# Performance work log

Hardware: AMD Instinct MI355X
Metric: run time of the kernel (lower is better)

Reference implementation:

```python
import jax, jax.numpy as jnp
import numpy as np

B, S, D, U, A = 8, 2048, 1024, 1024, 4  # batch, seq, input_dim, units, n_activations


def setup_inputs() -> dict:
    key = jax.random.key(0)
    ks = jax.random.split(key, 6)
    scale_w = (6.0 / (D + U)) ** 0.5  # glorot_uniform
    scale_wf = (6.0 / (U + A)) ** 0.5
    scale_wa = (6.0 / (D + A)) ** 0.5
    return {
        "x": jax.random.normal(ks[0], (B, S, D), dtype=jnp.float32),
        "w": jax.random.uniform(ks[1], (D, U), jnp.float32, -scale_w, scale_w),
        "b": jnp.zeros((U,), jnp.float32),
        "wf": jax.random.uniform(ks[2], (U, A), jnp.float32, -scale_wf, scale_wf),
        "bf": jnp.zeros((U, A), jnp.float32),
        "w_att": jax.random.uniform(ks[3], (D, A), jnp.float32, -scale_wa, scale_wa),
        "b_att": jnp.zeros((A,), jnp.float32),
    }


def reference(x, w, b, wf, bf, w_att, b_att):
    # weighted_sum: [B,S,U]
    ws = jnp.einsum('bsd,du->bsu', x, w) + b
    # broadcast per-activation affine: [B,S,U,A]
    wa = ws[..., None] * wf + bf
    acts = [
        jax.nn.relu(wa[..., 0]),
        jax.nn.sigmoid(wa[..., 1]),
        jnp.tanh(wa[..., 2]),
        jax.nn.gelu(wa[..., 3], approximate=False),  # tf.nn.gelu default is exact
    ]
    result_activations = jnp.stack(acts, axis=-1)  # [B,S,U,A]
    # attention over activations: [B,S,A]
    attn = jax.nn.softmax(jnp.einsum('bsd,da->bsa', x, w_att) + b_att, axis=-1)
    # weighted reduce over activation axis -> [B,S,U]
    out = jnp.einsum('bsua,bsa->bsu', result_activations, attn)
    return out
```

## Files before the change

### kernel.cpp

```cpp
#include <hip/hip_runtime.h>
#include <hip/hip_bf16.h>
#include <cstdint>

#define B_ 8
#define S_ 2048
#define D_ 1024
#define U_ 1024
#define M_ (B_ * S_)

typedef __bf16 bf16x8 __attribute__((ext_vector_type(8)));
typedef float  f32x4  __attribute__((ext_vector_type(4)));

__device__ __forceinline__ uint16_t f2bf(float f) {
  uint32_t u = __builtin_bit_cast(uint32_t, f);
  u += 0x7fffu + ((u >> 16) & 1u);
  return (uint16_t)(u >> 16);
}

__device__ __forceinline__ void async_copy16(const void* g, void* l) {
  typedef const __attribute__((address_space(1))) uint8_t* gp_t;
  typedef __attribute__((address_space(3))) uint8_t* lp_t;
  __builtin_amdgcn_global_load_lds((gp_t)(uintptr_t)g,
                                   (lp_t)(uint32_t)(uintptr_t)l, 16, 0, 0);
}

__global__ __launch_bounds__(256) void k_prep(
    const float* __restrict__ x, const float* __restrict__ w_att,
    const float* __restrict__ b_att, const float* __restrict__ w,
    uint16_t* __restrict__ x_bf, float* __restrict__ attn,
    uint16_t* __restrict__ wt) {
  __shared__ float tile[32][33];
  const int bid = blockIdx.x;
  if (bid < M_ / 4) {
    const int wave = threadIdx.x >> 6, lane = threadIdx.x & 63;
    const int row = bid * 4 + wave;
    const float4* xr = reinterpret_cast<const float4*>(x + (size_t)row * D_);
    const float4* wa4 = reinterpret_cast<const float4*>(w_att);
    float4 v[4];
#pragma unroll
    for (int i = 0; i < 4; i++) v[i] = xr[lane + 64 * i];
    float4 p = {0.f, 0.f, 0.f, 0.f};
#pragma unroll
    for (int i = 0; i < 4; i++) {
      const int base = 4 * (lane + 64 * i);
      const float xe[4] = {v[i].x, v[i].y, v[i].z, v[i].w};
#pragma unroll
      for (int c = 0; c < 4; c++) {
        float4 wv = wa4[base + c];
        p.x = fmaf(xe[c], wv.x, p.x);
        p.y = fmaf(xe[c], wv.y, p.y);
        p.z = fmaf(xe[c], wv.z, p.z);
        p.w = fmaf(xe[c], wv.w, p.w);
      }
      ushort4 hb;
      hb.x = f2bf(v[i].x); hb.y = f2bf(v[i].y);
      hb.z = f2bf(v[i].z); hb.w = f2bf(v[i].w);
      reinterpret_cast<ushort4*>(x_bf + (size_t)row * D_)[lane + 64 * i] = hb;
    }
#pragma unroll
    for (int off = 32; off > 0; off >>= 1) {
      p.x += __shfl_xor(p.x, off);
      p.y += __shfl_xor(p.y, off);
      p.z += __shfl_xor(p.z, off);
      p.w += __shfl_xor(p.w, off);
    }
    if (lane == 0) {
      float l0 = p.x + b_att[0], l1 = p.y + b_att[1];
      float l2 = p.z + b_att[2], l3 = p.w + b_att[3];
      float mx = fmaxf(fmaxf(l0, l1), fmaxf(l2, l3));
      float e0 = __expf(l0 - mx), e1 = __expf(l1 - mx);
      float e2 = __expf(l2 - mx), e3 = __expf(l3 - mx);
      float inv = __builtin_amdgcn_rcpf(e0 + e1 + e2 + e3);
      reinterpret_cast<float4*>(attn)[row] =
          make_float4(e0 * inv, e1 * inv, e2 * inv, e3 * inv);
    }
  } else {
    const int wid = bid - M_ / 4;
    const int t = threadIdx.x;
    const int tx = t & 31, ty = t >> 5;
    const int c0 = (wid & 31) * 32;
    const int r0 = (wid >> 5) * 32;
#pragma unroll
    for (int i = 0; i < 4; i++) {
      int r = ty + i * 8;
      tile[r][tx] = w[(size_t)(r0 + r) * U_ + c0 + tx];
    }
    __syncthreads();
#pragma unroll
    for (int i = 0; i < 4; i++) {
      int r = ty + i * 8;
      wt[(size_t)(c0 + r) * D_ + r0 + tx] = f2bf(tile[tx][r]);
    }
  }
}

#define BM 128
#define BN 128
#define BK 64

__global__ __launch_bounds__(256, 4) void k_gemm_ep(
    const uint16_t* __restrict__ xbf, const uint16_t* __restrict__ wt,
    const float* __restrict__ bias, const float* __restrict__ wf,
    const float* __restrict__ bfb, const float* __restrict__ attn,
    float* __restrict__ out) {
  __shared__ uint16_t As[BM * BK];
  __shared__ uint16_t Bs[BN * BK];

  const int t = threadIdx.x;
  const int wave = t >> 6, lane = t & 63;
  const int l16 = lane & 15, quad = lane >> 4;
  const int wm = wave >> 1, wn = wave & 1;
  const int m0 = blockIdx.y * BM;
  const int n0 = blockIdx.x * BN;

  const uint16_t* aBase = xbf + (size_t)m0 * D_;
  const uint16_t* bBase = wt + (size_t)n0 * D_;

  f32x4 acc[4][4] = {};

  for (int k0 = 0; k0 < D_; k0 += BK) {
#pragma unroll
    for (int it = 0; it < 4; it++) {
      int c = t + it * 256;
      int r = c >> 3;
      int cs = c & 7;
      int gc = cs ^ (r & 7);
      async_copy16(aBase + (size_t)r * D_ + k0 + gc * 8, (uint8_t*)As + c * 16);
      async_copy16(bBase + (size_t)r * D_ + k0 + gc * 8, (uint8_t*)Bs + c * 16);
    }
    __syncthreads();

#pragma unroll
    for (int ks = 0; ks < 2; ks++) {
      const int kcb = ks * 4;
      bf16x8 af[4], bfr[4];
#pragma unroll
      for (int i = 0; i < 4; i++) {
        int r = wm * 64 + i * 16 + l16;
        int cs = (kcb + quad) ^ (r & 7);
        af[i] = *reinterpret_cast<const bf16x8*>(&As[r * BK + cs * 8]);
      }
#pragma unroll
      for (int j = 0; j < 4; j++) {
        int n = wn * 64 + j * 16 + l16;
        int cs = (kcb + quad) ^ (n & 7);
        bfr[j] = *reinterpret_cast<const bf16x8*>(&Bs[n * BK + cs * 8]);
      }
#pragma unroll
      for (int i = 0; i < 4; i++)
#pragma unroll
        for (int j = 0; j < 4; j++)
          acc[i][j] = __builtin_amdgcn_mfma_f32_16x16x32_bf16(af[i], bfr[j], acc[i][j], 0, 0, 0);
    }
    __syncthreads();
  }

  float bu[4];
  float4 wf4[4], bf4[4];
#pragma unroll
  for (int j = 0; j < 4; j++) {
    int u = n0 + wn * 64 + j * 16 + l16;
    bu[j] = bias[u];
    wf4[j] = reinterpret_cast<const float4*>(wf)[u];
    bf4[j] = reinterpret_cast<const float4*>(bfb)[u];
  }
#pragma unroll
  for (int i = 0; i < 4; i++) {
#pragma unroll
    for (int r = 0; r < 4; r++) {
      int mg = m0 + wm * 64 + i * 16 + quad * 4 + r;
      float4 at = reinterpret_cast<const float4*>(attn)[mg];
      float* orow = out + (size_t)mg * U_;
#pragma unroll
      for (int j = 0; j < 4; j++) {
        int u = n0 + wn * 64 + j * 16 + l16;
        float wsv = acc[i][j][r] + bu[j];
        float wa0 = fmaf(wsv, wf4[j].x, bf4[j].x);
        float wa1 = fmaf(wsv, wf4[j].y, bf4[j].y);
        float wa2 = fmaf(wsv, wf4[j].z, bf4[j].z);
        float wa3 = fmaf(wsv, wf4[j].w, bf4[j].w);
        float a_relu = fmaxf(wa0, 0.f);
        float a_sig = __builtin_amdgcn_rcpf(
            1.f + __builtin_amdgcn_exp2f(-1.4426950409f * wa1));
        float a_tanh = fmaf(2.f, __builtin_amdgcn_rcpf(
            1.f + __builtin_amdgcn_exp2f(-2.8853900818f * wa2)), -1.f);
        float y = wa3 * fmaf(0.044715f, wa3 * wa3, 1.f);
        float a_gelu = wa3 * __builtin_amdgcn_rcpf(
            1.f + __builtin_amdgcn_exp2f(-2.302207929f * y));
        orow[u] = at.x * a_relu + at.y * a_sig + at.z * a_tanh + at.w * a_gelu;
      }
    }
  }
}

extern "C" void kernel_launch(void* const* d_in, const int* in_sizes, int n_in,
                              void* d_out, int out_size, void* d_ws, size_t ws_size,
                              hipStream_t stream) {
  const float* x     = (const float*)d_in[0];
  const float* w     = (const float*)d_in[1];
  const float* b     = (const float*)d_in[2];
  const float* wf    = (const float*)d_in[3];
  const float* bfb   = (const float*)d_in[4];
  const float* w_att = (const float*)d_in[5];
  const float* b_att = (const float*)d_in[6];
  float* out = (float*)d_out;

  char* ws = (char*)d_ws;
  uint16_t* x_bf = (uint16_t*)ws;
  uint16_t* w_t  = (uint16_t*)(ws + ((size_t)32 << 20));
  float*    attn = (float*)(ws + ((size_t)34 << 20));

  k_prep<<<dim3(M_ / 4 + 1024), 256, 0, stream>>>(x, w_att, b_att, w, x_bf, attn, w_t);
  k_gemm_ep<<<dim3(U_ / BN, M_ / BM), 256, 0, stream>>>(x_bf, w_t, b, wf, bfb, attn, out);
}
```

Baseline: 178.8 us.

## Fuse prep and GEMM kernels into one persistent launch with grid barrier

```diff
diff --git a/kernel.cpp b/kernel.cpp
--- a/kernel.cpp
+++ b/kernel.cpp
@@ -8,6 +8,11 @@
 #define U_ 1024
 #define M_ (B_ * S_)
 
+#define BM 128
+#define BN 128
+#define BK 64
+#define NBLK 1024
+
 typedef __bf16 bf16x8 __attribute__((ext_vector_type(8)));
 typedef float  f32x4  __attribute__((ext_vector_type(4)));
 
@@ -24,62 +29,38 @@
                                    (lp_t)(uint32_t)(uintptr_t)l, 16, 0, 0);
 }
 
-__global__ __launch_bounds__(256) void k_prep(
-    const float* __restrict__ x, const float* __restrict__ w_att,
-    const float* __restrict__ b_att, const float* __restrict__ w,
-    uint16_t* __restrict__ x_bf, float* __restrict__ attn,
-    uint16_t* __restrict__ wt) {
-  __shared__ float tile[32][33];
+__device__ __forceinline__ void grid_barrier(unsigned* ctr) {
+  __syncthreads();
+  if (threadIdx.x == 0) {
+    __hip_atomic_fetch_add(ctr, 1u, __ATOMIC_ACQ_REL, __HIP_MEMORY_SCOPE_AGENT);
+    while (__hip_atomic_load(ctr, __ATOMIC_ACQUIRE, __HIP_MEMORY_SCOPE_AGENT) <
+           (unsigned)NBLK) {
+      __builtin_amdgcn_s_sleep(8);
+    }
+  }
+  __syncthreads();
+}
+
+__global__ __launch_bounds__(256, 4) void k_fused(
+    const float* __restrict__ x, const float* __restrict__ w,
+    const float* __restrict__ w_att, const float* __restrict__ b_att,
+    const float* __restrict__ bias, const float* __restrict__ wf,
+    const float* __restrict__ bfb,
+    uint16_t* __restrict__ x_bf, uint16_t* __restrict__ wt,
+    float* __restrict__ attn, unsigned* __restrict__ bar,
+    float* __restrict__ out) {
+  __shared__ uint16_t As[BM * BK];
+  __shared__ uint16_t Bs[BN * BK];
+
   const int bid = blockIdx.x;
-  if (bid < M_ / 4) {
-    const int wave = threadIdx.x >> 6, lane = threadIdx.x & 63;
-    const int row = bid * 4 + wave;
-    const float4* xr = reinterpret_cast<const float4*>(x + (size_t)row * D_);
-    const float4* wa4 = reinterpret_cast<const float4*>(w_att);
-    float4 v[4];
-#pragma unroll
-    for (int i = 0; i < 4; i++) v[i] = xr[lane + 64 * i];
-    float4 p = {0.f, 0.f, 0.f, 0.f};
-#pragma unroll
-    for (int i = 0; i < 4; i++) {
-      const int base = 4 * (lane + 64 * i);
-      const float xe[4] = {v[i].x, v[i].y, v[i].z, v[i].w};
-#pragma unroll
-      for (int c = 0; c < 4; c++) {
-        float4 wv = wa4[base + c];
-        p.x = fmaf(xe[c], wv.x, p.x);
-        p.y = fmaf(xe[c], wv.y, p.y);
-        p.z = fmaf(xe[c], wv.z, p.z);
-        p.w = fmaf(xe[c], wv.w, p.w);
-      }
-      ushort4 hb;
-      hb.x = f2bf(v[i].x); hb.y = f2bf(v[i].y);
-      hb.z = f2bf(v[i].z); hb.w = f2bf(v[i].w);
-      reinterpret_cast<ushort4*>(x_bf + (size_t)row * D_)[lane + 64 * i] = hb;
-    }
-#pragma unroll
-    for (int off = 32; off > 0; off >>= 1) {
-      p.x += __shfl_xor(p.x, off);
-      p.y += __shfl_xor(p.y, off);
-      p.z += __shfl_xor(p.z, off);
-      p.w += __shfl_xor(p.w, off);
-    }
-    if (lane == 0) {
-      float l0 = p.x + b_att[0], l1 = p.y + b_att[1];
-      float l2 = p.z + b_att[2], l3 = p.w + b_att[3];
-      float mx = fmaxf(fmaxf(l0, l1), fmaxf(l2, l3));
-      float e0 = __expf(l0 - mx), e1 = __expf(l1 - mx);
-      float e2 = __expf(l2 - mx), e3 = __expf(l3 - mx);
-      float inv = __builtin_amdgcn_rcpf(e0 + e1 + e2 + e3);
-      reinterpret_cast<float4*>(attn)[row] =
-          make_float4(e0 * inv, e1 * inv, e2 * inv, e3 * inv);
-    }
-  } else {
-    const int wid = bid - M_ / 4;
-    const int t = threadIdx.x;
+  const int t = threadIdx.x;
+  const int wave = t >> 6, lane = t & 63;
+
+  {
+    float(*tile)[33] = reinterpret_cast<float(*)[33]>(As);
     const int tx = t & 31, ty = t >> 5;
-    const int c0 = (wid & 31) * 32;
-    const int r0 = (wid >> 5) * 32;
+    const int c0 = (bid & 31) * 32;
+    const int r0 = (bid >> 5) * 32;
 #pragma unroll
     for (int i = 0; i < 4; i++) {
       int r = ty + i * 8;
@@ -92,28 +73,62 @@
       wt[(size_t)(c0 + r) * D_ + r0 + tx] = f2bf(tile[tx][r]);
     }
   }
-}
-
-#define BM 128
-#define BN 128
-#define BK 64
-
-__global__ __launch_bounds__(256, 4) void k_gemm_ep(
-    const uint16_t* __restrict__ xbf, const uint16_t* __restrict__ wt,
-    const float* __restrict__ bias, const float* __restrict__ wf,
-    const float* __restrict__ bfb, const float* __restrict__ attn,
-    float* __restrict__ out) {
-  __shared__ uint16_t As[BM * BK];
-  __shared__ uint16_t Bs[BN * BK];
-
-  const int t = threadIdx.x;
-  const int wave = t >> 6, lane = t & 63;
+
+  {
+    const float4* wa4 = reinterpret_cast<const float4*>(w_att);
+#pragma unroll 1
+    for (int rr = 0; rr < 4; rr++) {
+      const int row = bid * 16 + wave * 4 + rr;
+      const float4* xr = reinterpret_cast<const float4*>(x + (size_t)row * D_);
+      float4 v[4];
+#pragma unroll
+      for (int i = 0; i < 4; i++) v[i] = xr[lane + 64 * i];
+      float4 p = {0.f, 0.f, 0.f, 0.f};
+#pragma unroll
+      for (int i = 0; i < 4; i++) {
+        const int base = 4 * (lane + 64 * i);
+        const float xe[4] = {v[i].x, v[i].y, v[i].z, v[i].w};
+#pragma unroll
+        for (int c = 0; c < 4; c++) {
+          float4 wv = wa4[base + c];
+          p.x = fmaf(xe[c], wv.x, p.x);
+          p.y = fmaf(xe[c], wv.y, p.y);
+          p.z = fmaf(xe[c], wv.z, p.z);
+          p.w = fmaf(xe[c], wv.w, p.w);
+        }
+        ushort4 hb;
+        hb.x = f2bf(v[i].x); hb.y = f2bf(v[i].y);
+        hb.z = f2bf(v[i].z); hb.w = f2bf(v[i].w);
+        reinterpret_cast<ushort4*>(x_bf + (size_t)row * D_)[lane + 64 * i] = hb;
+      }
+#pragma unroll
+      for (int off = 32; off > 0; off >>= 1) {
+        p.x += __shfl_xor(p.x, off);
+        p.y += __shfl_xor(p.y, off);
+        p.z += __shfl_xor(p.z, off);
+        p.w += __shfl_xor(p.w, off);
+      }
+      if (lane == 0) {
+        float l0 = p.x + b_att[0], l1 = p.y + b_att[1];
+        float l2 = p.z + b_att[2], l3 = p.w + b_att[3];
+        float mx = fmaxf(fmaxf(l0, l1), fmaxf(l2, l3));
+        float e0 = __expf(l0 - mx), e1 = __expf(l1 - mx);
+        float e2 = __expf(l2 - mx), e3 = __expf(l3 - mx);
+        float inv = __builtin_amdgcn_rcpf(e0 + e1 + e2 + e3);
+        reinterpret_cast<float4*>(attn)[row] =
+            make_float4(e0 * inv, e1 * inv, e2 * inv, e3 * inv);
+      }
+    }
+  }
+
+  grid_barrier(bar);
+
   const int l16 = lane & 15, quad = lane >> 4;
   const int wm = wave >> 1, wn = wave & 1;
-  const int m0 = blockIdx.y * BM;
-  const int n0 = blockIdx.x * BN;
-
-  const uint16_t* aBase = xbf + (size_t)m0 * D_;
+  const int m0 = (bid >> 3) * BM;
+  const int n0 = (bid & 7) * BN;
+
+  const uint16_t* aBase = x_bf + (size_t)m0 * D_;
   const uint16_t* bBase = wt + (size_t)n0 * D_;
 
   f32x4 acc[4][4] = {};
@@ -209,7 +224,9 @@
   uint16_t* x_bf = (uint16_t*)ws;
   uint16_t* w_t  = (uint16_t*)(ws + ((size_t)32 << 20));
   float*    attn = (float*)(ws + ((size_t)34 << 20));
-
-  k_prep<<<dim3(M_ / 4 + 1024), 256, 0, stream>>>(x, w_att, b_att, w, x_bf, attn, w_t);
-  k_gemm_ep<<<dim3(U_ / BN, M_ / BM), 256, 0, stream>>>(x_bf, w_t, b, wf, bfb, attn, out);
-}
+  unsigned* bar  = (unsigned*)(ws + ((size_t)35 << 20));
+
+  hipMemsetAsync(bar, 0, 64, stream);
+  k_fused<<<dim3(NBLK), 256, 0, stream>>>(x, w, w_att, b_att, b, wf, bfb,
+                                          x_bf, w_t, attn, bar, out);
+}
```

Measured after the change: 324.5 us. 1.81x slower.
